# Kernel optimization log

Hardware: AMD Instinct MI355X
Metric: run time of the kernel (lower is better)

Reference implementation:

```python
import jax, jax.numpy as jnp
import numpy as np

KNN = 30
NUM_RBFS = 16
MIN_RBF, MAX_RBF = 2.0, 22.0
SPREAD = (MAX_RBF - MIN_RBF) / NUM_RBFS
D_MODEL = 128
A = 4                      # 3 backbone atoms + virtual (Ca+Cb) atom
E_DIM = NUM_RBFS * A * A   # 256, matches LayerNorm(num_rbfs*4*4)
Z, N = 2, 4096


def setup_inputs() -> dict:
    key = jax.random.key(0)
    k1, k2 = jax.random.split(key)
    # coords spread out so neighbor distances land across the RBF range [2, 22]
    C = jax.random.normal(k1, (Z, N, A, 3), jnp.float32) * 5.0
    node_mask = jnp.zeros((Z, N), bool)  # True = padded residue
    rbf_centers = jnp.linspace(MIN_RBF, MAX_RBF, NUM_RBFS).astype(jnp.float32)
    ln_gamma = jnp.ones((E_DIM,), jnp.float32)
    ln_beta = jnp.zeros((E_DIM,), jnp.float32)
    W = (jax.random.normal(k2, (E_DIM, D_MODEL), jnp.float32) / np.sqrt(E_DIM))
    b = jnp.zeros((D_MODEL,), jnp.float32)
    return {"C": C, "node_mask": node_mask, "rbf_centers": rbf_centers,
            "ln_gamma": ln_gamma, "ln_beta": ln_beta, "W": W, "b": b}


def _layernorm(x, g, b2, eps=1e-5):
    mu = jnp.mean(x, -1, keepdims=True)
    var = jnp.mean((x - mu) ** 2, -1, keepdims=True)
    return (x - mu) * jax.lax.rsqrt(var + eps) * g + b2


def _safe_dist(sq):
    pos = sq > 0
    return jnp.where(pos, jnp.sqrt(jnp.where(pos, sq, 1.0)), 0.0)


def _neighbors(Ca, node_mask):
    Zb, Nn, _ = Ca.shape
    # squared pairwise distances; topk on sq-dist == topk on dist (monotone)
    sq = jnp.sum((Ca[:, None, :, :] - Ca[:, :, None, :]) ** 2, -1)  # [Z,N,N]
    sq = jnp.where((sq == 0) | node_mask[:, :, None], jnp.inf, sq)
    neg, idx = jax.lax.top_k(-sq, KNN)  # K smallest
    sqv = -neg                           # squared topk distances
    nbr_mask = jnp.take_along_axis(
        jnp.broadcast_to(node_mask[:, :, None], (Zb, Nn, KNN)), idx, axis=1)
    # dist != 0 and dist < 12  <=>  sq != 0 and sq < 144
    edge_mask = (~(node_mask[:, :, None] | nbr_mask)) & (sqv != 0) & (sqv < 144.0)
    node_idxs = jnp.arange(Nn)[None, :, None]
    Kidx = jnp.where(edge_mask, idx, node_idxs)
    return Kidx, edge_mask


def _edges(C, Kidx, rbf_centers, ln_gamma, ln_beta, W, b):
    Zb, Nn, Kk = Kidx.shape
    CK = jax.vmap(lambda c, k: c[k])(C, Kidx)                     # [Z,N,K,A,3]
    diff = C[:, :, None, :, None, :] - CK[:, :, :, None, :, :]    # [Z,N,K,A,A,3]
    d = _safe_dist(jnp.sum(diff ** 2, -1))                        # [Z,N,K,A,A]
    rbf = jnp.exp(-((d[..., None] - rbf_centers) ** 2) / (SPREAD ** 2))
    E = rbf.reshape(Zb, Nn, Kk, -1)                               # [Z,N,K,256]
    return _layernorm(E, ln_gamma, ln_beta) @ W + b               # [Z,N,K,128]


def reference(C, node_mask, rbf_centers, ln_gamma, ln_beta, W, b):
    Ca = C[:, :, 1, :]  # alpha carbon
    Kidx, edge_mask = _neighbors(Ca, node_mask)
    E = _edges(C, Kidx, rbf_centers, ln_gamma, ln_beta, W, b)
    return E, Kidx, edge_mask
```

## Files before the change

### kernel.cpp

```cpp
#include <hip/hip_runtime.h>
#include <math.h>

#define ZB 2
#define NN 4096
#define KNNv 30
#define EDIM 256
#define DM 128
#define BINS 4096
#define CAP 2048

typedef __attribute__((ext_vector_type(8))) short bf16x8;
typedef __attribute__((ext_vector_type(4))) float fx4;

#define ELN_STR 264

static __device__ inline unsigned short f2bf(float f) {
    unsigned int u = __float_as_uint(f);
    unsigned int r = u + 0x7fffu + ((u >> 16) & 1u);
    return (unsigned short)(r >> 16);
}

__global__ __launch_bounds__(256) void caprep_kernel(
    const float* __restrict__ C, float4* __restrict__ Ca4)
{
    int tid = blockIdx.x * 256 + threadIdx.x;
    if (tid < ZB * NN) {
        const float* p = C + (size_t)tid * 12 + 3;
        Ca4[tid] = make_float4(p[0], p[1], p[2], 0.0f);
    }
}

__global__ __launch_bounds__(256) void wprep_kernel(
    const float* __restrict__ W, const float* __restrict__ gamma_,
    unsigned short* __restrict__ Wt)
{
    int base = blockIdx.x * 1024 + threadIdx.x;
    #pragma unroll
    for (int q = 0; q < 4; ++q) {
        int idx = base + q * 256;
        int k = idx >> 7, n = idx & 127;
        Wt[n * 256 + k] = f2bf(W[idx] * gamma_[k]);
    }
}

__global__ __launch_bounds__(128) void biasprep_kernel(
    const float* __restrict__ W, const float* __restrict__ beta_,
    const float* __restrict__ bias, float* __restrict__ bias2)
{
    int n = threadIdx.x;
    float acc = bias[n];
    #pragma unroll 8
    for (int k = 0; k < EDIM; ++k) acc += beta_[k] * W[k * 128 + n];
    bias2[n] = acc;
}

__global__ __launch_bounds__(256) void knn_kernel(
    const float4* __restrict__ Ca4,
    const unsigned char* __restrict__ node_mask,
    float* __restrict__ out_kidx,
    float* __restrict__ out_emask)
{
    __shared__ unsigned int hist[BINS];
    __shared__ unsigned long long buf[CAP];
    __shared__ unsigned int wsum[4];
    __shared__ int s_cut;
    __shared__ unsigned int s_m;
    __shared__ unsigned long long sel[KNNv];

    const int bi = blockIdx.x;
    const int z  = bi >> 12;
    const int i  = bi & (NN - 1);
    const int t  = threadIdx.x;

    for (int q = t; q < BINS; q += 256) hist[q] = 0u;
    if (t == 0) s_m = 0u;
    __syncthreads();

    const float4 me = Ca4[bi];
    const float xi = me.x, yi = me.y, zi = me.z;
    const bool mask_i = node_mask[bi] != 0;
    const float4* Cz = Ca4 + ((size_t)z << 12);

    unsigned int keys[16];
    #pragma unroll
    for (int q = 0; q < 16; ++q) {
        const int j = q * 256 + t;
        float4 p = Cz[j];
        float dx = p.x - xi, dy = p.y - yi, dz = p.z - zi;
        float s = dx * dx + dy * dy + dz * dz;
        if (s == 0.0f || mask_i) s = __builtin_inff();
        unsigned int k = __float_as_uint(s);
        keys[q] = k;
        atomicAdd(&hist[k >> 20], 1u);
    }
    __syncthreads();

    unsigned int cnt[16]; unsigned int Tsum = 0;
    #pragma unroll
    for (int q = 0; q < 16; ++q) { cnt[q] = hist[t * 16 + q]; Tsum += cnt[q]; }
    unsigned int incl = Tsum;
    #pragma unroll
    for (int off = 1; off < 64; off <<= 1) {
        unsigned int v = __shfl_up(incl, off);
        if ((t & 63) >= off) incl += v;
    }
    if ((t & 63) == 63) wsum[t >> 6] = incl;
    __syncthreads();
    unsigned int woff = 0;
    for (int w = 0; w < (t >> 6); ++w) woff += wsum[w];
    unsigned int run = woff + incl - Tsum;
    #pragma unroll
    for (int q = 0; q < 16; ++q) {
        unsigned int c = cnt[q];
        if (run < KNNv && run + c >= KNNv) s_cut = t * 16 + q;
        run += c;
    }
    __syncthreads();

    const int cutbin = s_cut;
    #pragma unroll
    for (int q = 0; q < 16; ++q) {
        unsigned int k = keys[q];
        if ((int)(k >> 20) <= cutbin) {
            unsigned int pos = atomicAdd(&s_m, 1u);
            if (pos < CAP)
                buf[pos] = ((unsigned long long)k << 32) | (unsigned int)(q * 256 + t);
        }
    }
    __syncthreads();
    unsigned int M = s_m; if (M > CAP) M = CAP;

    for (unsigned int c = t; c < M; c += 256) {
        unsigned long long mev = buf[c];
        unsigned int r = 0;
        for (unsigned int o = 0; o < M; ++o) r += (buf[o] < mev) ? 1u : 0u;
        if (r < KNNv) sel[r] = mev;
    }
    __syncthreads();

    if (t < KNNv) {
        unsigned long long p = sel[t];
        unsigned int k = (unsigned int)(p >> 32);
        int j = (int)(p & 0xffffffffu);
        float sv = __uint_as_float(k);
        bool nb = node_mask[(size_t)z * NN + j] != 0;
        bool em = (!mask_i && !nb) && (sv != 0.0f) && (sv < 144.0f);
        int kv = em ? j : i;
        size_t o = (size_t)bi * KNNv + t;
        out_kidx[o]  = (float)kv;
        out_emask[o] = em ? 1.0f : 0.0f;
    }
}

__global__ __launch_bounds__(256) void edge_kernel(
    const float* __restrict__ C,
    const float* __restrict__ kidxf,
    const float* __restrict__ centers,
    const unsigned short* __restrict__ Wt,
    const float* __restrict__ bias2,
    float* __restrict__ outE)
{
    __shared__ unsigned short Eln[64 * ELN_STR];
    const int t = threadIdx.x;
    const long g0 = (long)blockIdx.x * 64;

    {
        const int e   = t >> 2;
        const int sub = t & 3;
        const long g = g0 + e;
        const int z   = (int)(g / (NN * KNNv));
        const int rem = (int)(g - (long)z * NN * KNNv);
        const int i   = rem / KNNv;
        const int j   = (int)kidxf[g];

        const float* Ci = C + (((size_t)z * NN + i) * 4 + sub) * 3;
        const float ax = Ci[0], ay = Ci[1], az = Ci[2];
        const float* Cj = C + ((size_t)z * NN + j) * 12;
        float d[4];
        #pragma unroll
        for (int b = 0; b < 4; ++b) {
            float dx = ax - Cj[b * 3 + 0];
            float dy = ay - Cj[b * 3 + 1];
            float dz = az - Cj[b * 3 + 2];
            float s = dx * dx + dy * dy + dz * dz;
            d[b] = s > 0.0f ? sqrtf(s) : 0.0f;
        }
        float cen[16];
        #pragma unroll
        for (int r = 0; r < 16; ++r) cen[r] = centers[r];

        float vals[64];
        float sum = 0.f, sumsq = 0.f;
        #pragma unroll
        for (int b = 0; b < 4; ++b) {
            #pragma unroll
            for (int r = 0; r < 16; ++r) {
                float dd = d[b] - cen[r];
                float v = __expf(dd * dd * -0.64f);
                vals[b * 16 + r] = v;
                sum += v; sumsq += v * v;
            }
        }
        sum   += __shfl_xor(sum, 1);   sum   += __shfl_xor(sum, 2);
        sumsq += __shfl_xor(sumsq, 1); sumsq += __shfl_xor(sumsq, 2);
        const float mu   = sum * (1.0f / 256.0f);
        const float var  = sumsq * (1.0f / 256.0f) - mu * mu;
        const float rstd = rsqrtf(var + 1e-5f);
        #pragma unroll
        for (int w = 0; w < 8; ++w) {
            bf16x8 pk;
            #pragma unroll
            for (int v = 0; v < 8; ++v)
                pk[v] = (short)f2bf((vals[w * 8 + v] - mu) * rstd);
            *(bf16x8*)&Eln[e * ELN_STR + sub * 64 + w * 8] = pk;
        }
    }
    __syncthreads();

    {
        const int lane = t & 63;
        const int wv   = t >> 6;
        const int quad = lane >> 4;
        const int l15  = lane & 15;
        const int n0   = wv * 32;

        bf16x8 Bf[2][8];
        #pragma unroll
        for (int nt = 0; nt < 2; ++nt)
            #pragma unroll
            for (int ks = 0; ks < 8; ++ks)
                Bf[nt][ks] = *(const bf16x8*)(Wt + (size_t)(n0 + nt * 16 + l15) * 256
                                                 + ks * 32 + quad * 8);

        fx4 acc[4][2];
        #pragma unroll
        for (int mt = 0; mt < 4; ++mt)
            #pragma unroll
            for (int nt = 0; nt < 2; ++nt)
                acc[mt][nt] = (fx4){0.f, 0.f, 0.f, 0.f};

        #pragma unroll
        for (int ks = 0; ks < 8; ++ks) {
            bf16x8 Af[4];
            #pragma unroll
            for (int mt = 0; mt < 4; ++mt)
                Af[mt] = *(const bf16x8*)&Eln[(mt * 16 + l15) * ELN_STR + ks * 32 + quad * 8];
            #pragma unroll
            for (int mt = 0; mt < 4; ++mt) {
                acc[mt][0] = __builtin_amdgcn_mfma_f32_16x16x32_bf16(Af[mt], Bf[0][ks], acc[mt][0], 0, 0, 0);
                acc[mt][1] = __builtin_amdgcn_mfma_f32_16x16x32_bf16(Af[mt], Bf[1][ks], acc[mt][1], 0, 0, 0);
            }
        }

        const float bb0 = bias2[n0 + l15];
        const float bb1 = bias2[n0 + 16 + l15];
        #pragma unroll
        for (int mt = 0; mt < 4; ++mt) {
            #pragma unroll
            for (int r = 0; r < 4; ++r) {
                const long row = g0 + mt * 16 + quad * 4 + r;
                float* orow = outE + (size_t)row * DM;
                orow[n0 + l15]      = acc[mt][0][r] + bb0;
                orow[n0 + 16 + l15] = acc[mt][1][r] + bb1;
            }
        }
    }
}

extern "C" void kernel_launch(void* const* d_in, const int* in_sizes, int n_in,
                              void* d_out, int out_size, void* d_ws, size_t ws_size,
                              hipStream_t stream) {
    const float* C          = (const float*)d_in[0];
    const unsigned char* nm = (const unsigned char*)d_in[1];
    const float* centers    = (const float*)d_in[2];
    const float* gamma_     = (const float*)d_in[3];
    const float* beta_      = (const float*)d_in[4];
    const float* W          = (const float*)d_in[5];
    const float* bias       = (const float*)d_in[6];

    float* out = (float*)d_out;
    const size_t nE = (size_t)ZB * NN * KNNv * DM;
    const size_t nK = (size_t)ZB * NN * KNNv;
    float* outE = out;
    float* outK = out + nE;
    float* outM = outK + nK;

    unsigned short* Wt   = (unsigned short*)d_ws;
    float*          bias2 = (float*)((char*)d_ws + 65536);
    float4*         Ca4  = (float4*)((char*)d_ws + 66048);

    caprep_kernel<<<32, 256, 0, stream>>>(C, Ca4);
    wprep_kernel<<<32, 256, 0, stream>>>(W, gamma_, Wt);
    biasprep_kernel<<<1, 128, 0, stream>>>(W, beta_, bias, bias2);
    knn_kernel<<<ZB * NN, 256, 0, stream>>>(Ca4, nm, outK, outM);
    edge_kernel<<<(int)(nK / 64), 256, 0, stream>>>(C, outK, centers, Wt, bias2, outE);
}
```

Before: 242.4 us.

## Replace KNN histogram with fixed threshold counts, merge prep kernels, vectorize neighbor loads

The KNN kernel drops the 4096-bin shared histogram and its prefix scan. It counts candidates below six fixed squared-distance thresholds using wave reductions, then picks the smallest threshold that holds at least K candidates. Candidates beyond 144 are irrelevant because those edges are masked, so missing slots get filled with self index and zero mask. This removes the shared-memory atomics, the histogram clear and one barrier, but it risks overflowing the candidate buffer or slowing the rank sort when the threshold lets in many points. The three prep kernels are merged into one launch, and the edge kernel loads neighbor coordinates as float4s.

```diff
diff --git a/kernel.cpp b/kernel.cpp
--- a/kernel.cpp
+++ b/kernel.cpp
@@ -6,8 +6,8 @@
 #define KNNv 30
 #define EDIM 256
 #define DM 128
-#define BINS 4096
-#define CAP 2048
+#define CAP2 2048
+#define NLV 6
 
 typedef __attribute__((ext_vector_type(8))) short bf16x8;
 typedef __attribute__((ext_vector_type(4))) float fx4;
@@ -20,38 +20,39 @@
     return (unsigned short)(r >> 16);
 }
 
-__global__ __launch_bounds__(256) void caprep_kernel(
-    const float* __restrict__ C, float4* __restrict__ Ca4)
+__global__ __launch_bounds__(256) void prep_kernel(
+    const float* __restrict__ C,
+    const float* __restrict__ W, const float* __restrict__ gamma_,
+    const float* __restrict__ beta_, const float* __restrict__ bias,
+    float4* __restrict__ Ca4, unsigned short* __restrict__ Wt,
+    float* __restrict__ bias2)
 {
-    int tid = blockIdx.x * 256 + threadIdx.x;
-    if (tid < ZB * NN) {
+    __shared__ float red[256];
+    const int b = blockIdx.x;
+    const int t = threadIdx.x;
+
+    if (b < 32) {
+        int tid = b * 256 + t;
         const float* p = C + (size_t)tid * 12 + 3;
         Ca4[tid] = make_float4(p[0], p[1], p[2], 0.0f);
-    }
-}
-
-__global__ __launch_bounds__(256) void wprep_kernel(
-    const float* __restrict__ W, const float* __restrict__ gamma_,
-    unsigned short* __restrict__ Wt)
-{
-    int base = blockIdx.x * 1024 + threadIdx.x;
-    #pragma unroll
-    for (int q = 0; q < 4; ++q) {
-        int idx = base + q * 256;
-        int k = idx >> 7, n = idx & 127;
-        Wt[n * 256 + k] = f2bf(W[idx] * gamma_[k]);
-    }
-}
-
-__global__ __launch_bounds__(128) void biasprep_kernel(
-    const float* __restrict__ W, const float* __restrict__ beta_,
-    const float* __restrict__ bias, float* __restrict__ bias2)
-{
-    int n = threadIdx.x;
-    float acc = bias[n];
-    #pragma unroll 8
-    for (int k = 0; k < EDIM; ++k) acc += beta_[k] * W[k * 128 + n];
-    bias2[n] = acc;
+    } else if (b < 64) {
+        int base = (b - 32) * 1024 + t;
+        #pragma unroll
+        for (int q = 0; q < 4; ++q) {
+            int idx = base + q * 256;
+            int k = idx >> 7, n = idx & 127;
+            Wt[n * 256 + k] = f2bf(W[idx] * gamma_[k]);
+        }
+    } else {
+        const int n = t & 127, half = t >> 7;
+        float acc = (half == 0) ? bias[n] : 0.0f;
+        const int k0 = half * 128;
+        #pragma unroll 8
+        for (int k = k0; k < k0 + 128; ++k) acc += beta_[k] * W[k * 128 + n];
+        red[t] = acc;
+        __syncthreads();
+        if (t < 128) bias2[n] = red[t] + red[t + 128];
+    }
 }
 
 __global__ __launch_bounds__(256) void knn_kernel(
@@ -60,28 +61,27 @@
     float* __restrict__ out_kidx,
     float* __restrict__ out_emask)
 {
-    __shared__ unsigned int hist[BINS];
-    __shared__ unsigned long long buf[CAP];
-    __shared__ unsigned int wsum[4];
-    __shared__ int s_cut;
+    __shared__ unsigned long long buf[CAP2];
+    __shared__ unsigned long long sel[KNNv];
+    __shared__ unsigned int wred[4 * NLV];
     __shared__ unsigned int s_m;
-    __shared__ unsigned long long sel[KNNv];
 
     const int bi = blockIdx.x;
     const int z  = bi >> 12;
     const int i  = bi & (NN - 1);
     const int t  = threadIdx.x;
-
-    for (int q = t; q < BINS; q += 256) hist[q] = 0u;
+    const int lane = t & 63;
+    const int wv   = t >> 6;
+
     if (t == 0) s_m = 0u;
-    __syncthreads();
 
     const float4 me = Ca4[bi];
     const float xi = me.x, yi = me.y, zi = me.z;
     const bool mask_i = node_mask[bi] != 0;
     const float4* Cz = Ca4 + ((size_t)z << 12);
 
-    unsigned int keys[16];
+    float sq[16];
+    unsigned int c0 = 0, c1 = 0, c2 = 0, c3 = 0, c4 = 0, c5 = 0;
     #pragma unroll
     for (int q = 0; q < 16; ++q) {
         const int j = q * 256 + t;
@@ -89,46 +89,46 @@
         float dx = p.x - xi, dy = p.y - yi, dz = p.z - zi;
         float s = dx * dx + dy * dy + dz * dz;
         if (s == 0.0f || mask_i) s = __builtin_inff();
-        unsigned int k = __float_as_uint(s);
-        keys[q] = k;
-        atomicAdd(&hist[k >> 20], 1u);
+        sq[q] = s;
+        c0 += (s < 4.0f);  c1 += (s < 8.0f);  c2 += (s < 18.0f);
+        c3 += (s < 40.0f); c4 += (s < 90.0f); c5 += (s < 144.0f);
+    }
+
+    unsigned int cc[NLV] = {c0, c1, c2, c3, c4, c5};
+    #pragma unroll
+    for (int lv = 0; lv < NLV; ++lv) {
+        unsigned int v = cc[lv];
+        v += __shfl_xor(v, 1);  v += __shfl_xor(v, 2);  v += __shfl_xor(v, 4);
+        v += __shfl_xor(v, 8);  v += __shfl_xor(v, 16); v += __shfl_xor(v, 32);
+        if (lane == 0) wred[wv * NLV + lv] = v;
     }
     __syncthreads();
 
-    unsigned int cnt[16]; unsigned int Tsum = 0;
+    unsigned int tot[NLV];
     #pragma unroll
-    for (int q = 0; q < 16; ++q) { cnt[q] = hist[t * 16 + q]; Tsum += cnt[q]; }
-    unsigned int incl = Tsum;
-    #pragma unroll
-    for (int off = 1; off < 64; off <<= 1) {
-        unsigned int v = __shfl_up(incl, off);
-        if ((t & 63) >= off) incl += v;
-    }
-    if ((t & 63) == 63) wsum[t >> 6] = incl;
-    __syncthreads();
-    unsigned int woff = 0;
-    for (int w = 0; w < (t >> 6); ++w) woff += wsum[w];
-    unsigned int run = woff + incl - Tsum;
+    for (int lv = 0; lv < NLV; ++lv)
+        tot[lv] = wred[0 * NLV + lv] + wred[1 * NLV + lv]
+                + wred[2 * NLV + lv] + wred[3 * NLV + lv];
+
+    float T = 144.0f;
+    if      (tot[0] >= KNNv) T = 4.0f;
+    else if (tot[1] >= KNNv) T = 8.0f;
+    else if (tot[2] >= KNNv) T = 18.0f;
+    else if (tot[3] >= KNNv) T = 40.0f;
+    else if (tot[4] >= KNNv) T = 90.0f;
+
     #pragma unroll
     for (int q = 0; q < 16; ++q) {
-        unsigned int c = cnt[q];
-        if (run < KNNv && run + c >= KNNv) s_cut = t * 16 + q;
-        run += c;
+        float s = sq[q];
+        if (s < T) {
+            unsigned int pos = atomicAdd(&s_m, 1u);
+            if (pos < CAP2)
+                buf[pos] = ((unsigned long long)__float_as_uint(s) << 32)
+                         | (unsigned int)(q * 256 + t);
+        }
     }
     __syncthreads();
-
-    const int cutbin = s_cut;
-    #pragma unroll
-    for (int q = 0; q < 16; ++q) {
-        unsigned int k = keys[q];
-        if ((int)(k >> 20) <= cutbin) {
-            unsigned int pos = atomicAdd(&s_m, 1u);
-            if (pos < CAP)
-                buf[pos] = ((unsigned long long)k << 32) | (unsigned int)(q * 256 + t);
-        }
-    }
-    __syncthreads();
-    unsigned int M = s_m; if (M > CAP) M = CAP;
+    unsigned int M = s_m; if (M > CAP2) M = CAP2;
 
     for (unsigned int c = t; c < M; c += 256) {
         unsigned long long mev = buf[c];
@@ -139,16 +139,22 @@
     __syncthreads();
 
     if (t < KNNv) {
-        unsigned long long p = sel[t];
-        unsigned int k = (unsigned int)(p >> 32);
-        int j = (int)(p & 0xffffffffu);
-        float sv = __uint_as_float(k);
-        bool nb = node_mask[(size_t)z * NN + j] != 0;
-        bool em = (!mask_i && !nb) && (sv != 0.0f) && (sv < 144.0f);
-        int kv = em ? j : i;
+        int kv; float emf;
+        if ((unsigned int)t < M) {
+            unsigned long long p = sel[t];
+            unsigned int kbits = (unsigned int)(p >> 32);
+            int j = (int)(p & 0xffffffffu);
+            float sv = __uint_as_float(kbits);
+            bool nb = node_mask[(size_t)z * NN + j] != 0;
+            bool em = (!mask_i && !nb) && (sv != 0.0f) && (sv < 144.0f);
+            kv = em ? j : i;
+            emf = em ? 1.0f : 0.0f;
+        } else {
+            kv = i; emf = 0.0f;
+        }
         size_t o = (size_t)bi * KNNv + t;
         out_kidx[o]  = (float)kv;
-        out_emask[o] = em ? 1.0f : 0.0f;
+        out_emask[o] = emf;
     }
 }
 
@@ -175,13 +181,20 @@
 
         const float* Ci = C + (((size_t)z * NN + i) * 4 + sub) * 3;
         const float ax = Ci[0], ay = Ci[1], az = Ci[2];
-        const float* Cj = C + ((size_t)z * NN + j) * 12;
+        const float* Cjp = C + ((size_t)z * NN + j) * 12;
+        float4 q0 = *(const float4*)(Cjp);
+        float4 q1 = *(const float4*)(Cjp + 4);
+        float4 q2 = *(const float4*)(Cjp + 8);
+        const float jx[4] = {q0.x, q0.w, q1.z, q2.y};
+        const float jy[4] = {q0.y, q1.x, q1.w, q2.z};
+        const float jz[4] = {q0.z, q1.y, q2.x, q2.w};
+
         float d[4];
         #pragma unroll
         for (int b = 0; b < 4; ++b) {
-            float dx = ax - Cj[b * 3 + 0];
-            float dy = ay - Cj[b * 3 + 1];
-            float dz = az - Cj[b * 3 + 2];
+            float dx = ax - jx[b];
+            float dy = ay - jy[b];
+            float dz = az - jz[b];
             float s = dx * dx + dy * dy + dz * dz;
             d[b] = s > 0.0f ? sqrtf(s) : 0.0f;
         }
@@ -285,13 +298,11 @@
     float* outK = out + nE;
     float* outM = outK + nK;
 
-    unsigned short* Wt   = (unsigned short*)d_ws;
+    unsigned short* Wt    = (unsigned short*)d_ws;
     float*          bias2 = (float*)((char*)d_ws + 65536);
-    float4*         Ca4  = (float4*)((char*)d_ws + 66048);
-
-    caprep_kernel<<<32, 256, 0, stream>>>(C, Ca4);
-    wprep_kernel<<<32, 256, 0, stream>>>(W, gamma_, Wt);
-    biasprep_kernel<<<1, 128, 0, stream>>>(W, beta_, bias, bias2);
+    float4*         Ca4   = (float4*)((char*)d_ws + 66048);
+
+    prep_kernel<<<65, 256, 0, stream>>>(C, W, gamma_, beta_, bias, Ca4, Wt, bias2);
     knn_kernel<<<ZB * NN, 256, 0, stream>>>(Ca4, nm, outK, outM);
     edge_kernel<<<(int)(nK / 64), 256, 0, stream>>>(C, outK, centers, Wt, bias2, outE);
 }
```

Result: faster. 224.2 us (-7.5%).
